# Optimization experiments

Measured on AMD Instinct MI355X. Metric: run time of the kernel, lower is better.

The kernel has to match this reference:

```python
import jax, jax.numpy as jnp
import numpy as np

NUM_HEAD = 16
HEAD_DIM = 64
SEQ, BATCH, DMODEL = 2048, 2, 1024


def setup_inputs() -> dict:
    key = jax.random.key(0)
    ks = jax.random.split(key, 6)
    xavier = lambda k, shp: jax.random.uniform(
        k, shp, jnp.float32, -1.0, 1.0) * np.sqrt(6.0 / (shp[0] + shp[1]))
    query = jax.random.normal(ks[0], (SEQ, BATCH, DMODEL), jnp.float32)
    q_w = xavier(ks[1], (DMODEL, DMODEL))
    k_w = xavier(ks[2], (DMODEL, DMODEL))
    v_w = xavier(ks[3], (DMODEL, DMODEL))
    out_w = xavier(ks[4], (DMODEL, DMODEL))
    zeros = jnp.zeros((DMODEL,), jnp.float32)
    # causal mask: True = masked out (key position after query position)
    causal = jnp.triu(jnp.ones((SEQ, SEQ), bool), k=1)
    attn_mask = jnp.broadcast_to(causal, (BATCH, SEQ, SEQ))
    return {
        "query": query,
        "q_w": q_w, "q_b": zeros,
        "k_w": k_w, "k_b": zeros,
        "v_w": v_w, "v_b": zeros,
        "out_w": out_w, "out_b": zeros,
        "attn_mask": attn_mask,
    }


def reference(query, q_w, q_b, k_w, k_b, v_w, v_b, out_w, out_b, attn_mask):
    S, B, _ = query.shape
    H, Dh = NUM_HEAD, HEAD_DIM
    scale = 1.0 / np.sqrt(Dh)
    # self-attention: key = value = query
    q = (query @ q_w.T + q_b).reshape(S, B, H, Dh)
    k = (query @ k_w.T + k_b).reshape(S, B, H, Dh)
    v = (query @ v_w.T + v_b).reshape(S, B, H, Dh)
    # scores: [B, H, S(query), S(key)]
    scores = jnp.einsum('sbhd,tbhd->bhst', q, k) * scale
    scores = jnp.where(attn_mask[:, None, :, :], -jnp.inf, scores)
    attn = jax.nn.softmax(scores, axis=-1)
    # context: [S, B, H, Dh] -> [S, B, H*Dh]
    ctx = jnp.einsum('bhst,tbhd->sbhd', attn, v).reshape(S, B, H * Dh)
    return ctx @ out_w.T + out_b
```

## Files before the change

kernel.cpp:

```cpp
#include <hip/hip_runtime.h>
#include <hip/hip_bf16.h>

typedef __bf16 bf16;
typedef __attribute__((ext_vector_type(2))) __bf16 bf16x2;
typedef __attribute__((ext_vector_type(4))) __bf16 bf16x4;
typedef __attribute__((ext_vector_type(8))) __bf16 bf16x8;
typedef __attribute__((ext_vector_type(4))) float f32x4;

static_assert(sizeof(bf16x8) == 16, "bf16x8 must be 16B");

#define S_LEN 2048
#define BATCH_N 2
#define DM 1024
#define NHEAD 16
#define HDIM 64
#define LOG2E 1.44269504088896f

__device__ __forceinline__ void async_cp16(const void* g, void* l) {
    __builtin_amdgcn_global_load_lds(
        (const __attribute__((address_space(1))) void*)g,
        (__attribute__((address_space(3))) void*)l, 16, 0, 0);
}

__global__ __launch_bounds__(256)
void cvt_all(const float* __restrict__ q,
             const float* __restrict__ w0, const float* __restrict__ w1,
             const float* __restrict__ w2, const float* __restrict__ w3,
             bf16* __restrict__ Xb,
             bf16* __restrict__ W0, bf16* __restrict__ W1,
             bf16* __restrict__ W2, bf16* __restrict__ W3) {
    const int blk = blockIdx.x;
    const float* src;
    bf16* dst;
    size_t base;
    if (blk < 2048) {
        src = q; dst = Xb; base = (size_t)blk * 2048;
    } else {
        const int w = (blk - 2048) >> 9;
        const int r = (blk - 2048) & 511;
        base = (size_t)r * 2048;
        src = (w == 0) ? w0 : (w == 1) ? w1 : (w == 2) ? w2 : w3;
        dst = (w == 0) ? W0 : (w == 1) ? W1 : (w == 2) ? W2 : W3;
    }
    const size_t i = base + (size_t)threadIdx.x * 8;
    const f32x4 a = *(const f32x4*)(src + i);
    const f32x4 b = *(const f32x4*)(src + i + 4);
    bf16x8 r8;
    r8[0] = (bf16)a[0]; r8[1] = (bf16)a[1]; r8[2] = (bf16)a[2]; r8[3] = (bf16)a[3];
    r8[4] = (bf16)b[0]; r8[5] = (bf16)b[1]; r8[6] = (bf16)b[2]; r8[7] = (bf16)b[3];
    *(bf16x8*)(dst + i) = r8;
}

__device__ __forceinline__ void gemm_tile64(const bf16* __restrict__ A,
                                            const bf16* __restrict__ W,
                                            int row0, int col0, int Kdim,
                                            f32x4 acc[2][4]) {
    __shared__ bf16 As[64 * 32];
    __shared__ bf16 Bs[128 * 32];
    const int tid  = threadIdx.x;
    const int lane = tid & 63;
    const int wv   = tid >> 6;
    const int wr = wv >> 1, wc = wv & 1;
    const int qr = lane & 15, quad = lane >> 4;

    const int srow = wv * 16 + (lane >> 2);
    const int scol = (lane & 3) * 8;
    const bf16* Ap  = A + (size_t)(row0 + srow) * Kdim + scol;
    const bf16* Wp0 = W + (size_t)(col0 + srow) * Kdim + scol;
    const bf16* Wp1 = W + (size_t)(col0 + 64 + srow) * Kdim + scol;
    bf16* lA  = As + wv * 512;
    bf16* lB0 = Bs + wv * 512;
    bf16* lB1 = Bs + 64 * 32 + wv * 512;

    const f32x4 fzero = {0.f, 0.f, 0.f, 0.f};
    #pragma unroll
    for (int mi = 0; mi < 2; ++mi)
        #pragma unroll
        for (int ni = 0; ni < 4; ++ni)
            acc[mi][ni] = fzero;

    for (int k0 = 0; k0 < Kdim; k0 += 32) {
        __syncthreads();
        async_cp16(Ap + k0, lA);
        async_cp16(Wp0 + k0, lB0);
        async_cp16(Wp1 + k0, lB1);
        __syncthreads();

        bf16x8 af[2], bfr[4];
        #pragma unroll
        for (int mi = 0; mi < 2; ++mi)
            af[mi] = *(const bf16x8*)(As + (wr * 32 + mi * 16 + qr) * 32 + quad * 8);
        #pragma unroll
        for (int ni = 0; ni < 4; ++ni)
            bfr[ni] = *(const bf16x8*)(Bs + (wc * 64 + ni * 16 + qr) * 32 + quad * 8);
        #pragma unroll
        for (int mi = 0; mi < 2; ++mi)
            #pragma unroll
            for (int ni = 0; ni < 4; ++ni)
                acc[mi][ni] = __builtin_amdgcn_mfma_f32_16x16x32_bf16(
                    af[mi], bfr[ni], acc[mi][ni], 0, 0, 0);
    }
}

__global__ __launch_bounds__(256)
void qkv_kernel(const bf16* __restrict__ X,
                const bf16* __restrict__ Wq, const float* __restrict__ bq,
                const bf16* __restrict__ Wk, const float* __restrict__ bk,
                const bf16* __restrict__ Wv, const float* __restrict__ bv,
                bf16* __restrict__ Q, bf16* __restrict__ Kt, bf16* __restrict__ Vt) {
    const int mat  = blockIdx.z;
    const bf16*  W    = (mat == 0) ? Wq : (mat == 1) ? Wk : Wv;
    const float* bias = (mat == 0) ? bq : (mat == 1) ? bk : bv;
    const int col0 = blockIdx.x * 128;
    const int row0 = blockIdx.y * 64;

    f32x4 acc[2][4];
    gemm_tile64(X, W, row0, col0, DM, acc);

    const int lane = threadIdx.x & 63;
    const int wave = threadIdx.x >> 6;
    const int wr = wave >> 1, wc = wave & 1;
    const int qr = lane & 15, quad = lane >> 4;

    #pragma unroll
    for (int ni = 0; ni < 4; ++ni) {
        const int n  = col0 + wc * 64 + ni * 16 + qr;
        const float bn = bias[n];
        const int h = n >> 6, dh = n & 63;
        #pragma unroll
        for (int mi = 0; mi < 2; ++mi) {
            const int i0 = row0 + wr * 32 + mi * 16 + quad * 4;
            const float v0 = acc[mi][ni][0] + bn;
            const float v1 = acc[mi][ni][1] + bn;
            const float v2 = acc[mi][ni][2] + bn;
            const float v3 = acc[mi][ni][3] + bn;
            if (mat == 2) {
                const int s0 = i0 >> 1;
                bf16x2 e0 = {(bf16)v0, (bf16)v2};
                bf16x2 e1 = {(bf16)v1, (bf16)v3};
                *(bf16x2*)(Vt + ((size_t)h * HDIM + dh) * S_LEN + s0) = e0;
                *(bf16x2*)(Vt + ((size_t)(NHEAD + h) * HDIM + dh) * S_LEN + s0) = e1;
            } else {
                #pragma unroll
                for (int r = 0; r < 4; ++r) {
                    const int i = i0 + r;
                    const int s = i >> 1, b = i & 1;
                    const float v = (r == 0) ? v0 : (r == 1) ? v1 : (r == 2) ? v2 : v3;
                    if (mat == 0) {
                        Q[((size_t)(b * NHEAD + h) * S_LEN + s) * HDIM + dh] =
                            (bf16)(v * (0.125f * LOG2E));
                    } else {
                        Kt[((size_t)(b * NHEAD + h) * S_LEN + s) * HDIM + dh] = (bf16)v;
                    }
                }
            }
        }
    }
}

#define PLD 40
#define PT  640
#define WAVE_P (8*PT)
#define RSTRIDE 36

#define MFMA(a, b, c) __builtin_amdgcn_mfma_f32_16x16x32_bf16(a, b, c, 0, 0, 0)
#define EX(x) __builtin_amdgcn_exp2f(x)

#define QK_TILE(j) \
    f32x4 sA##j = MFMA(k0, qlo##j, fzero); sA##j = MFMA(k1, qhi##j, sA##j); \
    f32x4 sB##j = MFMA(k2, qlo##j, fzero); sB##j = MFMA(k3, qhi##j, sB##j);

#define SFULL(j) do { \
    const float e0 = EX(sA##j[0]), e1 = EX(sA##j[1]), e2 = EX(sA##j[2]), e3 = EX(sA##j[3]); \
    const float f0 = EX(sB##j[0]), f1 = EX(sB##j[1]), f2 = EX(sB##j[2]), f3 = EX(sB##j[3]); \
    l##j += (e0 + e1 + e2 + e3) + (f0 + f1 + f2 + f3); \
    bf16x4 wa = {(bf16)e0, (bf16)e1, (bf16)e2, (bf16)e3}; \
    bf16x4 wb = {(bf16)f0, (bf16)f1, (bf16)f2, (bf16)f3}; \
    *(bf16x4*)(PB + (j) * PT + qr * PLD + quad * 4)      = wa; \
    *(bf16x4*)(PB + (j) * PT + qr * PLD + 16 + quad * 4) = wb; \
} while (0)

#define SMASK(j) do { \
    const int qrow = qb0 + 16 * (j) + qr; \
    const int ka = t * 32 + quad * 4; \
    const float e0 = (ka + 0  <= qrow) ? EX(sA##j[0]) : 0.f; \
    const float e1 = (ka + 1  <= qrow) ? EX(sA##j[1]) : 0.f; \
    const float e2 = (ka + 2  <= qrow) ? EX(sA##j[2]) : 0.f; \
    const float e3 = (ka + 3  <= qrow) ? EX(sA##j[3]) : 0.f; \
    const float f0 = (ka + 16 <= qrow) ? EX(sB##j[0]) : 0.f; \
    const float f1 = (ka + 17 <= qrow) ? EX(sB##j[1]) : 0.f; \
    const float f2 = (ka + 18 <= qrow) ? EX(sB##j[2]) : 0.f; \
    const float f3 = (ka + 19 <= qrow) ? EX(sB##j[3]) : 0.f; \
    l##j += (e0 + e1 + e2 + e3) + (f0 + f1 + f2 + f3); \
    bf16x4 wa = {(bf16)e0, (bf16)e1, (bf16)e2, (bf16)e3}; \
    bf16x4 wb = {(bf16)f0, (bf16)f1, (bf16)f2, (bf16)f3}; \
    *(bf16x4*)(PB + (j) * PT + qr * PLD + quad * 4)      = wa; \
    *(bf16x4*)(PB + (j) * PT + qr * PLD + 16 + quad * 4) = wb; \
} while (0)

__global__ __launch_bounds__(256)
void attn_kernel(const bf16* __restrict__ Q, const bf16* __restrict__ K,
                 const bf16* __restrict__ Vt, bf16* __restrict__ ctx) {
    __shared__ __align__(16) char smem[40960];
    const int lane = threadIdx.x & 63;
    const int wave = threadIdx.x >> 6;
    const int qr = lane & 15, quad = lane >> 4;
    const int bh = blockIdx.y;
    const int b = bh >> 4, h = bh & 15;
    const int qb0 = ((int)gridDim.x - 1 - (int)blockIdx.x) * 64;
    const int tdiag = qb0 >> 5;
    const int tmax  = tdiag + 1;

    const bf16* Qb = Q  + (size_t)bh * S_LEN * HDIM;
    const bf16* Kb = K  + (size_t)bh * S_LEN * HDIM;
    const bf16* Vb = Vt + (size_t)bh * HDIM * S_LEN;

    const bf16x8 qlo0 = *(const bf16x8*)(Qb + (size_t)(qb0 + qr) * HDIM + quad * 8);
    const bf16x8 qhi0 = *(const bf16x8*)(Qb + (size_t)(qb0 + qr) * HDIM + quad * 8 + 32);
    const bf16x8 qlo1 = *(const bf16x8*)(Qb + (size_t)(qb0 + 16 + qr) * HDIM + quad * 8);
    const bf16x8 qhi1 = *(const bf16x8*)(Qb + (size_t)(qb0 + 16 + qr) * HDIM + quad * 8 + 32);
    const bf16x8 qlo2 = *(const bf16x8*)(Qb + (size_t)(qb0 + 32 + qr) * HDIM + quad * 8);
    const bf16x8 qhi2 = *(const bf16x8*)(Qb + (size_t)(qb0 + 32 + qr) * HDIM + quad * 8 + 32);
    const bf16x8 qlo3 = *(const bf16x8*)(Qb + (size_t)(qb0 + 48 + qr) * HDIM + quad * 8);
    const bf16x8 qhi3 = *(const bf16x8*)(Qb + (size_t)(qb0 + 48 + qr) * HDIM + quad * 8 + 32);

    const f32x4 fzero = {0.f, 0.f, 0.f, 0.f};
    f32x4 o0_0 = fzero, o0_1 = fzero, o0_2 = fzero, o0_3 = fzero;
    f32x4 o1_0 = fzero, o1_1 = fzero, o1_2 = fzero, o1_3 = fzero;
    f32x4 o2_0 = fzero, o2_1 = fzero, o2_2 = fzero, o2_3 = fzero;
    f32x4 o3_0 = fzero, o3_1 = fzero, o3_2 = fzero, o3_3 = fzero;
    float l0 = 0.f, l1 = 0.f, l2 = 0.f, l3 = 0.f;
    bf16* Pw = (bf16*)smem + wave * WAVE_P;

    for (int t = wave, c = 0; t <= tmax; t += 4, ++c) {
        const bf16* kp = Kb + ((size_t)t * 32 + qr) * HDIM + quad * 8;
        const bf16x8 k0 = *(const bf16x8*)(kp);
        const bf16x8 k1 = *(const bf16x8*)(kp + 32);
        const bf16x8 k2 = *(const bf16x8*)(kp + 16 * HDIM);
        const bf16x8 k3 = *(const bf16x8*)(kp + 16 * HDIM + 32);
        const bf16* vp = Vb + (size_t)qr * S_LEN + t * 32 + quad * 8;
        const bf16x8 v0 = *(const bf16x8*)(vp);
        const bf16x8 v1 = *(const bf16x8*)(vp + 16 * S_LEN);
        const bf16x8 v2 = *(const bf16x8*)(vp + 32 * S_LEN);
        const bf16x8 v3 = *(const bf16x8*)(vp + 48 * S_LEN);
        bf16* PB = Pw + (c & 1) * (4 * PT);

        if (t < tdiag) {
            QK_TILE(0); SFULL(0);
            QK_TILE(1); SFULL(1);
            QK_TILE(2); SFULL(2);
            QK_TILE(3); SFULL(3);
        } else {
            QK_TILE(0); SMASK(0);
            QK_TILE(1); SMASK(1);
            QK_TILE(2); SMASK(2);
            QK_TILE(3); SMASK(3);
        }

        const bf16x8 pf0 = *(const bf16x8*)(PB + 0 * PT + qr * PLD + quad * 8);
        const bf16x8 pf1 = *(const bf16x8*)(PB + 1 * PT + qr * PLD + quad * 8);
        const bf16x8 pf2 = *(const bf16x8*)(PB + 2 * PT + qr * PLD + quad * 8);
        const bf16x8 pf3 = *(const bf16x8*)(PB + 3 * PT + qr * PLD + quad * 8);
        o0_0 = MFMA(v0, pf0, o0_0); o0_1 = MFMA(v1, pf0, o0_1);
        o0_2 = MFMA(v2, pf0, o0_2); o0_3 = MFMA(v3, pf0, o0_3);
        o1_0 = MFMA(v0, pf1, o1_0); o1_1 = MFMA(v1, pf1, o1_1);
        o1_2 = MFMA(v2, pf1, o1_2); o1_3 = MFMA(v3, pf1, o1_3);
        o2_0 = MFMA(v0, pf2, o2_0); o2_1 = MFMA(v1, pf2, o2_1);
        o2_2 = MFMA(v2, pf2, o2_2); o2_3 = MFMA(v3, pf2, o2_3);
        o3_0 = MFMA(v0, pf3, o3_0); o3_1 = MFMA(v1, pf3, o3_1);
        o3_2 = MFMA(v2, pf3, o3_2); o3_3 = MFMA(v3, pf3, o3_3);
    }

    __syncthreads();
    float* red = (float*)smem;
    if (wave != 0) {
        float* rp = red + ((size_t)(wave - 1) * 64 + lane) * RSTRIDE;
        *(f32x4*)(rp +  0) = o0_0; *(f32x4*)(rp +  4) = o0_1;
        *(f32x4*)(rp +  8) = o0_2; *(f32x4*)(rp + 12) = o0_3;
        *(f32x4*)(rp + 16) = o1_0; *(f32x4*)(rp + 20) = o1_1;
        *(f32x4*)(rp + 24) = o1_2; *(f32x4*)(rp + 28) = o1_3;
        rp[32] = l0; rp[33] = l1;
    }
    __syncthreads();
    if (wave == 0) {
        #pragma unroll
        for (int w = 0; w < 3; ++w) {
            const float* rp = red + ((size_t)w * 64 + lane) * RSTRIDE;
            o0_0 += *(const f32x4*)(rp +  0); o0_1 += *(const f32x4*)(rp +  4);
            o0_2 += *(const f32x4*)(rp +  8); o0_3 += *(const f32x4*)(rp + 12);
            o1_0 += *(const f32x4*)(rp + 16); o1_1 += *(const f32x4*)(rp + 20);
            o1_2 += *(const f32x4*)(rp + 24); o1_3 += *(const f32x4*)(rp + 28);
            l0 += rp[32]; l1 += rp[33];
        }
    }
    __syncthreads();
    if (wave != 0) {
        float* rp = red + ((size_t)(wave - 1) * 64 + lane) * RSTRIDE;
        *(f32x4*)(rp +  0) = o2_0; *(f32x4*)(rp +  4) = o2_1;
        *(f32x4*)(rp +  8) = o2_2; *(f32x4*)(rp + 12) = o2_3;
        *(f32x4*)(rp + 16) = o3_0; *(f32x4*)(rp + 20) = o3_1;
        *(f32x4*)(rp + 24) = o3_2; *(f32x4*)(rp + 28) = o3_3;
        rp[32] = l2; rp[33] = l3;
    }
    __syncthreads();
    if (wave == 0) {
        #pragma unroll
        for (int w = 0; w < 3; ++w) {
            const float* rp = red + ((size_t)w * 64 + lane) * RSTRIDE;
            o2_0 += *(const f32x4*)(rp +  0); o2_1 += *(const f32x4*)(rp +  4);
            o2_2 += *(const f32x4*)(rp +  8); o2_3 += *(const f32x4*)(rp + 12);
            o3_0 += *(const f32x4*)(rp + 16); o3_1 += *(const f32x4*)(rp + 20);
            o3_2 += *(const f32x4*)(rp + 24); o3_3 += *(const f32x4*)(rp + 28);
            l2 += rp[32]; l3 += rp[33];
        }
        l0 += __shfl_xor(l0, 16); l0 += __shfl_xor(l0, 32);
        l1 += __shfl_xor(l1, 16); l1 += __shfl_xor(l1, 32);
        l2 += __shfl_xor(l2, 16); l2 += __shfl_xor(l2, 32);
        l3 += __shfl_xor(l3, 16); l3 += __shfl_xor(l3, 32);
        const float inv0 = 1.f / l0, inv1 = 1.f / l1;
        const float inv2 = 1.f / l2, inv3 = 1.f / l3;

        #define OWRITE(ov, ni_, qrow_, inv_) do { \
            bf16x4 cc = {(bf16)(ov[0] * (inv_)), (bf16)(ov[1] * (inv_)), \
                         (bf16)(ov[2] * (inv_)), (bf16)(ov[3] * (inv_))}; \
            *(bf16x4*)(ctx + (size_t)((qrow_) * BATCH_N + b) * DM \
                       + h * 64 + (ni_) * 16 + quad * 4) = cc; \
        } while (0)
        OWRITE(o0_0, 0, qb0 + qr, inv0);      OWRITE(o0_1, 1, qb0 + qr, inv0);
        OWRITE(o0_2, 2, qb0 + qr, inv0);      OWRITE(o0_3, 3, qb0 + qr, inv0);
        OWRITE(o1_0, 0, qb0 + 16 + qr, inv1); OWRITE(o1_1, 1, qb0 + 16 + qr, inv1);
        OWRITE(o1_2, 2, qb0 + 16 + qr, inv1); OWRITE(o1_3, 3, qb0 + 16 + qr, inv1);
        OWRITE(o2_0, 0, qb0 + 32 + qr, inv2); OWRITE(o2_1, 1, qb0 + 32 + qr, inv2);
        OWRITE(o2_2, 2, qb0 + 32 + qr, inv2); OWRITE(o2_3, 3, qb0 + 32 + qr, inv2);
        OWRITE(o3_0, 0, qb0 + 48 + qr, inv3); OWRITE(o3_1, 1, qb0 + 48 + qr, inv3);
        OWRITE(o3_2, 2, qb0 + 48 + qr, inv3); OWRITE(o3_3, 3, qb0 + 48 + qr, inv3);
        #undef OWRITE
    }
}

__global__ __launch_bounds__(256)
void proj_kernel(const bf16* __restrict__ X, const bf16* __restrict__ W,
                 const float* __restrict__ bias, float* __restrict__ out) {
    const int col0 = blockIdx.x * 128;
    const int row0 = blockIdx.y * 64;
    f32x4 acc[2][4];
    gemm_tile64(X, W, row0, col0, DM, acc);

    const int lane = threadIdx.x & 63;
    const int wave = threadIdx.x >> 6;
    const int wr = wave >> 1, wc = wave & 1;
    const int qr = lane & 15, quad = lane >> 4;

    #pragma unroll
    for (int ni = 0; ni < 4; ++ni) {
        const int n = col0 + wc * 64 + ni * 16 + qr;
        const float bn = bias[n];
        #pragma unroll
        for (int mi = 0; mi < 2; ++mi) {
            #pragma unroll
            for (int r = 0; r < 4; ++r) {
                const int i = row0 + wr * 32 + mi * 16 + quad * 4 + r;
                out[(size_t)i * DM + n] = acc[mi][ni][r] + bn;
            }
        }
    }
}

extern "C" void kernel_launch(void* const* d_in, const int* in_sizes, int n_in,
                              void* d_out, int out_size, void* d_ws, size_t ws_size,
                              hipStream_t stream) {
    (void)in_sizes; (void)n_in; (void)out_size; (void)ws_size;
    const float* query = (const float*)d_in[0];
    const float* q_w   = (const float*)d_in[1];
    const float* q_b   = (const float*)d_in[2];
    const float* k_w   = (const float*)d_in[3];
    const float* k_b   = (const float*)d_in[4];
    const float* v_w   = (const float*)d_in[5];
    const float* v_b   = (const float*)d_in[6];
    const float* out_w = (const float*)d_in[7];
    const float* out_b = (const float*)d_in[8];

    char* ws = (char*)d_ws;
    bf16* Xb  = (bf16*)(ws);
    bf16* Wqb = (bf16*)(ws + ((size_t)8  << 20));
    bf16* Wkb = (bf16*)(ws + ((size_t)10 << 20));
    bf16* Wvb = (bf16*)(ws + ((size_t)12 << 20));
    bf16* Wob = (bf16*)(ws + ((size_t)14 << 20));
    bf16* Qb  = (bf16*)(ws + ((size_t)16 << 20));
    bf16* Kb  = (bf16*)(ws + ((size_t)24 << 20));
    bf16* Vt  = (bf16*)(ws + ((size_t)32 << 20));
    bf16* ctx = (bf16*)(ws + ((size_t)40 << 20));
    float* out = (float*)d_out;

    dim3 blk(256);
    cvt_all<<<dim3(2048 + 4 * 512), blk, 0, stream>>>(
        query, q_w, k_w, v_w, out_w, Xb, Wqb, Wkb, Wvb, Wob);

    qkv_kernel<<<dim3(DM / 128, (S_LEN * BATCH_N) / 64, 3), blk, 0, stream>>>(
        Xb, Wqb, q_b, Wkb, k_b, Wvb, v_b, Qb, Kb, Vt);
    attn_kernel<<<dim3(S_LEN / 64, BATCH_N * NHEAD), blk, 0, stream>>>(
        Qb, Kb, Vt, ctx);
    proj_kernel<<<dim3(DM / 128, (S_LEN * BATCH_N) / 64), blk, 0, stream>>>(
        ctx, Wob, out_b, out);
}
```

Measured before the change: 247.3 us.

## Enlarge GEMM tiles to 128x128 and prefetch K fragments in attention loop

The shared GEMM helper now computes 128x128 output tiles per block instead of 64x128, so each wave holds 4x4 accumulators and every loaded A/W tile feeds more MFMAs. The QKV and output projection grids are halved to match. In the attention kernel, K fragments for the next key tile are loaded into registers before the current step runs, using a two-register ping-pong. The double-buffered P scratch is reduced to a single buffer, which shrinks shared memory. The larger tiles raise register pressure and give the grid fewer blocks, and the single P buffer drops the previous double buffering.

```diff
diff --git a/kernel.cpp b/kernel.cpp
--- a/kernel.cpp
+++ b/kernel.cpp
@@ -51,11 +51,11 @@
     *(bf16x8*)(dst + i) = r8;
 }
 
-__device__ __forceinline__ void gemm_tile64(const bf16* __restrict__ A,
-                                            const bf16* __restrict__ W,
-                                            int row0, int col0, int Kdim,
-                                            f32x4 acc[2][4]) {
-    __shared__ bf16 As[64 * 32];
+__device__ __forceinline__ void gemm_tile(const bf16* __restrict__ A,
+                                          const bf16* __restrict__ W,
+                                          int row0, int col0, int Kdim,
+                                          f32x4 acc[4][4]) {
+    __shared__ bf16 As[128 * 32];
     __shared__ bf16 Bs[128 * 32];
     const int tid  = threadIdx.x;
     const int lane = tid & 63;
@@ -65,36 +65,37 @@
 
     const int srow = wv * 16 + (lane >> 2);
     const int scol = (lane & 3) * 8;
-    const bf16* Ap  = A + (size_t)(row0 + srow) * Kdim + scol;
-    const bf16* Wp0 = W + (size_t)(col0 + srow) * Kdim + scol;
-    const bf16* Wp1 = W + (size_t)(col0 + 64 + srow) * Kdim + scol;
-    bf16* lA  = As + wv * 512;
+    const bf16* Ap = A + (size_t)(row0 + srow) * Kdim + scol;
+    const bf16* Wp = W + (size_t)(col0 + srow) * Kdim + scol;
+    bf16* lA0 = As + wv * 512;
+    bf16* lA1 = As + 64 * 32 + wv * 512;
     bf16* lB0 = Bs + wv * 512;
     bf16* lB1 = Bs + 64 * 32 + wv * 512;
 
     const f32x4 fzero = {0.f, 0.f, 0.f, 0.f};
     #pragma unroll
-    for (int mi = 0; mi < 2; ++mi)
+    for (int mi = 0; mi < 4; ++mi)
         #pragma unroll
         for (int ni = 0; ni < 4; ++ni)
             acc[mi][ni] = fzero;
 
     for (int k0 = 0; k0 < Kdim; k0 += 32) {
         __syncthreads();
-        async_cp16(Ap + k0, lA);
-        async_cp16(Wp0 + k0, lB0);
-        async_cp16(Wp1 + k0, lB1);
+        async_cp16(Ap + k0, lA0);
+        async_cp16(Ap + (size_t)64 * Kdim + k0, lA1);
+        async_cp16(Wp + k0, lB0);
+        async_cp16(Wp + (size_t)64 * Kdim + k0, lB1);
         __syncthreads();
 
-        bf16x8 af[2], bfr[4];
-        #pragma unroll
-        for (int mi = 0; mi < 2; ++mi)
-            af[mi] = *(const bf16x8*)(As + (wr * 32 + mi * 16 + qr) * 32 + quad * 8);
+        bf16x8 af[4], bfr[4];
+        #pragma unroll
+        for (int mi = 0; mi < 4; ++mi)
+            af[mi] = *(const bf16x8*)(As + (wr * 64 + mi * 16 + qr) * 32 + quad * 8);
         #pragma unroll
         for (int ni = 0; ni < 4; ++ni)
             bfr[ni] = *(const bf16x8*)(Bs + (wc * 64 + ni * 16 + qr) * 32 + quad * 8);
         #pragma unroll
-        for (int mi = 0; mi < 2; ++mi)
+        for (int mi = 0; mi < 4; ++mi)
             #pragma unroll
             for (int ni = 0; ni < 4; ++ni)
                 acc[mi][ni] = __builtin_amdgcn_mfma_f32_16x16x32_bf16(
@@ -112,10 +113,10 @@
     const bf16*  W    = (mat == 0) ? Wq : (mat == 1) ? Wk : Wv;
     const float* bias = (mat == 0) ? bq : (mat == 1) ? bk : bv;
     const int col0 = blockIdx.x * 128;
-    const int row0 = blockIdx.y * 64;
-
-    f32x4 acc[2][4];
-    gemm_tile64(X, W, row0, col0, DM, acc);
+    const int row0 = blockIdx.y * 128;
+
+    f32x4 acc[4][4];
+    gemm_tile(X, W, row0, col0, DM, acc);
 
     const int lane = threadIdx.x & 63;
     const int wave = threadIdx.x >> 6;
@@ -128,8 +129,8 @@
         const float bn = bias[n];
         const int h = n >> 6, dh = n & 63;
         #pragma unroll
-        for (int mi = 0; mi < 2; ++mi) {
-            const int i0 = row0 + wr * 32 + mi * 16 + quad * 4;
+        for (int mi = 0; mi < 4; ++mi) {
+            const int i0 = row0 + wr * 64 + mi * 16 + quad * 4;
             const float v0 = acc[mi][ni][0] + bn;
             const float v1 = acc[mi][ni][1] + bn;
             const float v2 = acc[mi][ni][2] + bn;
@@ -160,15 +161,22 @@
 
 #define PLD 40
 #define PT  640
-#define WAVE_P (8*PT)
 #define RSTRIDE 36
 
 #define MFMA(a, b, c) __builtin_amdgcn_mfma_f32_16x16x32_bf16(a, b, c, 0, 0, 0)
 #define EX(x) __builtin_amdgcn_exp2f(x)
 
-#define QK_TILE(j) \
-    f32x4 sA##j = MFMA(k0, qlo##j, fzero); sA##j = MFMA(k1, qhi##j, sA##j); \
-    f32x4 sB##j = MFMA(k2, qlo##j, fzero); sB##j = MFMA(k3, qhi##j, sB##j);
+#define KLOAD(P, t_) do { \
+    const bf16* _kp = Kb + ((size_t)(t_) * 32 + qr) * HDIM + quad * 8; \
+    k##P##0 = *(const bf16x8*)(_kp); \
+    k##P##1 = *(const bf16x8*)(_kp + 32); \
+    k##P##2 = *(const bf16x8*)(_kp + 16 * HDIM); \
+    k##P##3 = *(const bf16x8*)(_kp + 16 * HDIM + 32); \
+} while (0)
+
+#define QK_TILE(P, j) \
+    f32x4 sA##j = MFMA(k##P##0, qlo##j, fzero); sA##j = MFMA(k##P##1, qhi##j, sA##j); \
+    f32x4 sB##j = MFMA(k##P##2, qlo##j, fzero); sB##j = MFMA(k##P##3, qhi##j, sB##j);
 
 #define SFULL(j) do { \
     const float e0 = EX(sA##j[0]), e1 = EX(sA##j[1]), e2 = EX(sA##j[2]), e3 = EX(sA##j[3]); \
@@ -176,13 +184,13 @@
     l##j += (e0 + e1 + e2 + e3) + (f0 + f1 + f2 + f3); \
     bf16x4 wa = {(bf16)e0, (bf16)e1, (bf16)e2, (bf16)e3}; \
     bf16x4 wb = {(bf16)f0, (bf16)f1, (bf16)f2, (bf16)f3}; \
-    *(bf16x4*)(PB + (j) * PT + qr * PLD + quad * 4)      = wa; \
-    *(bf16x4*)(PB + (j) * PT + qr * PLD + 16 + quad * 4) = wb; \
+    *(bf16x4*)(Pw + (j) * PT + qr * PLD + quad * 4)      = wa; \
+    *(bf16x4*)(Pw + (j) * PT + qr * PLD + 16 + quad * 4) = wb; \
 } while (0)
 
-#define SMASK(j) do { \
+#define SMASK(j, t_) do { \
     const int qrow = qb0 + 16 * (j) + qr; \
-    const int ka = t * 32 + quad * 4; \
+    const int ka = (t_) * 32 + quad * 4; \
     const float e0 = (ka + 0  <= qrow) ? EX(sA##j[0]) : 0.f; \
     const float e1 = (ka + 1  <= qrow) ? EX(sA##j[1]) : 0.f; \
     const float e2 = (ka + 2  <= qrow) ? EX(sA##j[2]) : 0.f; \
@@ -194,14 +202,45 @@
     l##j += (e0 + e1 + e2 + e3) + (f0 + f1 + f2 + f3); \
     bf16x4 wa = {(bf16)e0, (bf16)e1, (bf16)e2, (bf16)e3}; \
     bf16x4 wb = {(bf16)f0, (bf16)f1, (bf16)f2, (bf16)f3}; \
-    *(bf16x4*)(PB + (j) * PT + qr * PLD + quad * 4)      = wa; \
-    *(bf16x4*)(PB + (j) * PT + qr * PLD + 16 + quad * 4) = wb; \
+    *(bf16x4*)(Pw + (j) * PT + qr * PLD + quad * 4)      = wa; \
+    *(bf16x4*)(Pw + (j) * PT + qr * PLD + 16 + quad * 4) = wb; \
+} while (0)
+
+#define STEP(P, t_) do { \
+    const bf16* _vp = Vb + (size_t)qr * S_LEN + (t_) * 32 + quad * 8; \
+    const bf16x8 v0 = *(const bf16x8*)(_vp); \
+    const bf16x8 v1 = *(const bf16x8*)(_vp + 16 * S_LEN); \
+    const bf16x8 v2 = *(const bf16x8*)(_vp + 32 * S_LEN); \
+    const bf16x8 v3 = *(const bf16x8*)(_vp + 48 * S_LEN); \
+    if ((t_) < tdiag) { \
+        QK_TILE(P, 0); SFULL(0); \
+        QK_TILE(P, 1); SFULL(1); \
+        QK_TILE(P, 2); SFULL(2); \
+        QK_TILE(P, 3); SFULL(3); \
+    } else { \
+        QK_TILE(P, 0); SMASK(0, t_); \
+        QK_TILE(P, 1); SMASK(1, t_); \
+        QK_TILE(P, 2); SMASK(2, t_); \
+        QK_TILE(P, 3); SMASK(3, t_); \
+    } \
+    const bf16x8 pf0 = *(const bf16x8*)(Pw + 0 * PT + qr * PLD + quad * 8); \
+    const bf16x8 pf1 = *(const bf16x8*)(Pw + 1 * PT + qr * PLD + quad * 8); \
+    const bf16x8 pf2 = *(const bf16x8*)(Pw + 2 * PT + qr * PLD + quad * 8); \
+    const bf16x8 pf3 = *(const bf16x8*)(Pw + 3 * PT + qr * PLD + quad * 8); \
+    o0_0 = MFMA(v0, pf0, o0_0); o0_1 = MFMA(v1, pf0, o0_1); \
+    o0_2 = MFMA(v2, pf0, o0_2); o0_3 = MFMA(v3, pf0, o0_3); \
+    o1_0 = MFMA(v0, pf1, o1_0); o1_1 = MFMA(v1, pf1, o1_1); \
+    o1_2 = MFMA(v2, pf1, o1_2); o1_3 = MFMA(v3, pf1, o1_3); \
+    o2_0 = MFMA(v0, pf2, o2_0); o2_1 = MFMA(v1, pf2, o2_1); \
+    o2_2 = MFMA(v2, pf2, o2_2); o2_3 = MFMA(v3, pf2, o2_3); \
+    o3_0 = MFMA(v0, pf3, o3_0); o3_1 = MFMA(v1, pf3, o3_1); \
+    o3_2 = MFMA(v2, pf3, o3_2); o3_3 = MFMA(v3, pf3, o3_3); \
 } while (0)
 
 __global__ __launch_bounds__(256)
 void attn_kernel(const bf16* __restrict__ Q, const bf16* __restrict__ K,
                  const bf16* __restrict__ Vt, bf16* __restrict__ ctx) {
-    __shared__ __align__(16) char smem[40960];
+    __shared__ __align__(16) char smem[27648];
     const int lane = threadIdx.x & 63;
     const int wave = threadIdx.x >> 6;
     const int qr = lane & 15, quad = lane >> 4;
@@ -230,45 +269,27 @@
     f32x4 o2_0 = fzero, o2_1 = fzero, o2_2 = fzero, o2_3 = fzero;
     f32x4 o3_0 = fzero, o3_1 = fzero, o3_2 = fzero, o3_3 = fzero;
     float l0 = 0.f, l1 = 0.f, l2 = 0.f, l3 = 0.f;
-    bf16* Pw = (bf16*)smem + wave * WAVE_P;
-
-    for (int t = wave, c = 0; t <= tmax; t += 4, ++c) {
-        const bf16* kp = Kb + ((size_t)t * 32 + qr) * HDIM + quad * 8;
-        const bf16x8 k0 = *(const bf16x8*)(kp);
-        const bf16x8 k1 = *(const bf16x8*)(kp + 32);
-        const bf16x8 k2 = *(const bf16x8*)(kp + 16 * HDIM);
-        const bf16x8 k3 = *(const bf16x8*)(kp + 16 * HDIM + 32);
-        const bf16* vp = Vb + (size_t)qr * S_LEN + t * 32 + quad * 8;
-        const bf16x8 v0 = *(const bf16x8*)(vp);
-        const bf16x8 v1 = *(const bf16x8*)(vp + 16 * S_LEN);
-        const bf16x8 v2 = *(const bf16x8*)(vp + 32 * S_LEN);
-        const bf16x8 v3 = *(const bf16x8*)(vp + 48 * S_LEN);
-        bf16* PB = Pw + (c & 1) * (4 * PT);
-
-        if (t < tdiag) {
-            QK_TILE(0); SFULL(0);
-            QK_TILE(1); SFULL(1);
-            QK_TILE(2); SFULL(2);
-            QK_TILE(3); SFULL(3);
-        } else {
-            QK_TILE(0); SMASK(0);
-            QK_TILE(1); SMASK(1);
-            QK_TILE(2); SMASK(2);
-            QK_TILE(3); SMASK(3);
+    bf16* Pw = (bf16*)smem + wave * (4 * PT);
+    bf16x8 ka0, ka1, ka2, ka3, kb0, kb1, kb2, kb3;
+
+    {
+        int t = wave;
+        if (t <= tmax) {
+            KLOAD(a, t);
+            while (true) {
+                const int tn = t + 4;
+                const bool more = (tn <= tmax);
+                if (more) KLOAD(b, tn);
+                STEP(a, t);
+                if (!more) break;
+                const int tn2 = tn + 4;
+                const bool more2 = (tn2 <= tmax);
+                if (more2) KLOAD(a, tn2);
+                STEP(b, tn);
+                if (!more2) break;
+                t = tn2;
+            }
         }
-
-        const bf16x8 pf0 = *(const bf16x8*)(PB + 0 * PT + qr * PLD + quad * 8);
-        const bf16x8 pf1 = *(const bf16x8*)(PB + 1 * PT + qr * PLD + quad * 8);
-        const bf16x8 pf2 = *(const bf16x8*)(PB + 2 * PT + qr * PLD + quad * 8);
-        const bf16x8 pf3 = *(const bf16x8*)(PB + 3 * PT + qr * PLD + quad * 8);
-        o0_0 = MFMA(v0, pf0, o0_0); o0_1 = MFMA(v1, pf0, o0_1);
-        o0_2 = MFMA(v2, pf0, o0_2); o0_3 = MFMA(v3, pf0, o0_3);
-        o1_0 = MFMA(v0, pf1, o1_0); o1_1 = MFMA(v1, pf1, o1_1);
-        o1_2 = MFMA(v2, pf1, o1_2); o1_3 = MFMA(v3, pf1, o1_3);
-        o2_0 = MFMA(v0, pf2, o2_0); o2_1 = MFMA(v1, pf2, o2_1);
-        o2_2 = MFMA(v2, pf2, o2_2); o2_3 = MFMA(v3, pf2, o2_3);
-        o3_0 = MFMA(v0, pf3, o3_0); o3_1 = MFMA(v1, pf3, o3_1);
-        o3_2 = MFMA(v2, pf3, o3_2); o3_3 = MFMA(v3, pf3, o3_3);
     }
 
     __syncthreads();
@@ -342,9 +363,9 @@
 void proj_kernel(const bf16* __restrict__ X, const bf16* __restrict__ W,
                  const float* __restrict__ bias, float* __restrict__ out) {
     const int col0 = blockIdx.x * 128;
-    const int row0 = blockIdx.y * 64;
-    f32x4 acc[2][4];
-    gemm_tile64(X, W, row0, col0, DM, acc);
+    const int row0 = blockIdx.y * 128;
+    f32x4 acc[4][4];
+    gemm_tile(X, W, row0, col0, DM, acc);
 
     const int lane = threadIdx.x & 63;
     const int wave = threadIdx.x >> 6;
@@ -356,10 +377,10 @@
         const int n = col0 + wc * 64 + ni * 16 + qr;
         const float bn = bias[n];
         #pragma unroll
-        for (int mi = 0; mi < 2; ++mi) {
+        for (int mi = 0; mi < 4; ++mi) {
             #pragma unroll
             for (int r = 0; r < 4; ++r) {
-                const int i = row0 + wr * 32 + mi * 16 + quad * 4 + r;
+                const int i = row0 + wr * 64 + mi * 16 + quad * 4 + r;
                 out[(size_t)i * DM + n] = acc[mi][ni][r] + bn;
             }
         }
@@ -396,10 +417,10 @@
     cvt_all<<<dim3(2048 + 4 * 512), blk, 0, stream>>>(
         query, q_w, k_w, v_w, out_w, Xb, Wqb, Wkb, Wvb, Wob);
 
-    qkv_kernel<<<dim3(DM / 128, (S_LEN * BATCH_N) / 64, 3), blk, 0, stream>>>(
+    qkv_kernel<<<dim3(DM / 128, (S_LEN * BATCH_N) / 128, 3), blk, 0, stream>>>(
         Xb, Wqb, q_b, Wkb, k_b, Wvb, v_b, Qb, Kb, Vt);
     attn_kernel<<<dim3(S_LEN / 64, BATCH_N * NHEAD), blk, 0, stream>>>(
         Qb, Kb, Vt, ctx);
-    proj_kernel<<<dim3(DM / 128, (S_LEN * BATCH_N) / 64), blk, 0, stream>>>(
+    proj_kernel<<<dim3(DM / 128, (S_LEN * BATCH_N) / 128), blk, 0, stream>>>(
         ctx, Wob, out_b, out);
 }
```

Result: faster. 238.2 us (-3.7%).
